# Optimization experiments

Hardware: AMD Instinct MI355X
Metric: run time of the kernel (lower is better)

The kernel has to match this reference:

```python
import jax, jax.numpy as jnp
import numpy as np

N = 20000   # nodes per frame
T = 16      # frames
E = 320000  # edges per frame
C = 128     # in_channels
H = 128     # hidden_channels
P = 100000  # decode pairs


def setup_inputs() -> dict:
    key = jax.random.key(0)
    ks = jax.random.split(key, 12)
    s = 1.0 / np.sqrt(H)
    return {
        "x_seq": jax.random.normal(ks[0], (T, N, C), jnp.float32),
        "edge_index": jax.random.randint(ks[1], (T, 2, E), 0, N, jnp.int32),
        "edge_pairs": jax.random.randint(ks[2], (2, P), 0, N, jnp.int32),
        "W1": jax.random.normal(ks[3], (C, H), jnp.float32) * s,
        "b1": jnp.zeros((H,), jnp.float32),
        "W2": jax.random.normal(ks[4], (H, H), jnp.float32) * s,
        "b2": jnp.zeros((H,), jnp.float32),
        "W3": jax.random.normal(ks[5], (H, H), jnp.float32) * s,
        "b3": jnp.zeros((H,), jnp.float32),
        "w_ih": jax.random.normal(ks[6], (3 * H, H), jnp.float32) * s,
        "w_hh": jax.random.normal(ks[7], (3 * H, H), jnp.float32) * s,
        "b_ih": jnp.zeros((3 * H,), jnp.float32),
        "b_hh": jnp.zeros((3 * H,), jnp.float32),
    }


def _gcn(x, src, dst, W, b):
    # PyG GCNConv: h = x @ W; add self-loops; D^{-1/2}(A+I)D^{-1/2} aggregation; + b
    h = x @ W                                   # [N, H]
    ones = jnp.ones(src.shape[0], x.dtype)
    deg = jax.ops.segment_sum(ones, dst, num_segments=N) + 1.0  # self-loop included
    dinv = jax.lax.rsqrt(deg)
    norm = dinv[src] * dinv[dst]                # [E]
    agg = jax.ops.segment_sum(h[src] * norm[:, None], dst, num_segments=N)
    agg = agg + h * (dinv * dinv)[:, None]      # self-loop message (norm = 1/deg)
    return agg + b


def reference(x_seq, edge_index, edge_pairs, W1, b1, W2, b2, W3, b3,
              w_ih, w_hh, b_ih, b_hh):
    def frame(_, inp):
        x, ei = inp
        src, dst = ei[0], ei[1]
        h = jax.nn.relu(_gcn(x, src, dst, W1, b1))
        h = jax.nn.relu(_gcn(h, src, dst, W2, b2))
        h = _gcn(h, src, dst, W3, b3)
        return None, h

    _, feats = jax.lax.scan(frame, None, (x_seq, edge_index))  # [T, N, H]

    # single-layer torch GRU over time; only final hidden state needed
    def gru_step(hprev, x_t):
        gi = x_t @ w_ih.T + b_ih                # [N, 3H]
        gh = hprev @ w_hh.T + b_hh
        i_r, i_z, i_n = jnp.split(gi, 3, axis=1)
        h_r, h_z, h_n = jnp.split(gh, 3, axis=1)
        r = jax.nn.sigmoid(i_r + h_r)
        z = jax.nn.sigmoid(i_z + h_z)
        n = jnp.tanh(i_n + r * h_n)
        h_new = (1.0 - z) * n + z * hprev
        return h_new, None

    h0 = jnp.zeros((N, H), x_seq.dtype)
    h_last, _ = jax.lax.scan(gru_step, h0, feats)  # [N, H]

    zs = h_last[edge_pairs[0]]                  # [P, H]
    zd = h_last[edge_pairs[1]]
    return jnp.sum(zs * zd, axis=1)             # [P]
```

## Files before the change

### kernel.cpp

```cpp
#include <hip/hip_runtime.h>
#include <hip/hip_bf16.h>

#define NN 20000
#define TT 16
#define EE 320000
#define CC 128
#define HH 128
#define PP 100000
#define QN (NN / 4)

typedef float  f32x4  __attribute__((ext_vector_type(4)));
typedef unsigned short ushort8v __attribute__((ext_vector_type(8)));
typedef unsigned u32x4 __attribute__((ext_vector_type(4)));
typedef _Float16 h2v __attribute__((ext_vector_type(2)));
typedef _Float16 h4v __attribute__((ext_vector_type(4)));
typedef _Float16 f16x8 __attribute__((ext_vector_type(8)));

union pk16 { unsigned u; _Float16 h[2]; };


__global__ void hist_all_k(const int* __restrict__ edge_index, int* __restrict__ cnt_all) {
    int b = blockIdx.x;
    int f = b & 15, chunk = b >> 4;
    const int* dst = edge_index + (size_t)f * 2 * EE + EE;
    int* cnt = cnt_all + f * NN;
    int base = chunk * 1024 + threadIdx.x;
#pragma unroll
    for (int i = 0; i < 4; ++i) {
        int e = base + i * 256;
        if (e < EE) {
            int d = __builtin_nontemporal_load(dst + e);
            atomicAdd(&cnt[d], 1);
        }
    }
}

__global__ __launch_bounds__(1024) void scan_all_k(const int* __restrict__ cnt_all,
                                                   int* __restrict__ offs_all,
                                                   float* __restrict__ dinv_all,
                                                   int* __restrict__ cursor_all) {
    __shared__ int part[1024];
    int f = blockIdx.x;
    const int* cnt = cnt_all + f * NN;
    int* offs = offs_all + f * (NN + 1);
    int t = threadIdx.x;
    int base = t * 20;
    int vals[20];
    int s = 0;
#pragma unroll
    for (int i = 0; i < 20; ++i) {
        int idx = base + i;
        int v = (idx < NN) ? cnt[idx] : 0;
        vals[i] = v; s += v;
    }
    part[t] = s;
    __syncthreads();
    for (int off = 1; off < 1024; off <<= 1) {
        int v = (t >= off) ? part[t - off] : 0;
        __syncthreads();
        part[t] += v;
        __syncthreads();
    }
    int run = part[t] - s;
#pragma unroll
    for (int i = 0; i < 20; ++i) {
        int idx = base + i;
        if (idx < NN) {
            offs[idx] = run;
            cursor_all[f * NN + idx] = f * EE + run;
            dinv_all[f * NN + idx] = rsqrtf((float)vals[i] + 1.0f);
            run += vals[i];
        }
    }
    if (t == 0) offs[NN] = EE;
}

__global__ void fill_all_k(const int* __restrict__ edge_index,
                           int* __restrict__ cursor_all,
                           unsigned short* __restrict__ csr_all) {
    int b = blockIdx.x;
    int f = b & 15, chunk = b >> 4;
    const int* src = edge_index + (size_t)f * 2 * EE;
    const int* dst = src + EE;
    int* cur = cursor_all + f * NN;
    int base = chunk * 1024 + threadIdx.x;
#pragma unroll
    for (int i = 0; i < 4; ++i) {
        int e = base + i * 256;
        if (e < EE) {
            int d = __builtin_nontemporal_load(dst + e);
            int s = __builtin_nontemporal_load(src + e);
            int pos = atomicAdd(&cur[d], 1);
            csr_all[pos] = (unsigned short)s;
        }
    }
}

__global__ void wprep_t_k(const float* __restrict__ W,
                          _Float16* __restrict__ oh,
                          _Float16* __restrict__ ol) {
    int i = blockIdx.x * blockDim.x + threadIdx.x;
    if (i >= 128 * 128) return;
    int n = i >> 7, k = i & 127;
    float v = W[k * 128 + n];
    _Float16 h = (_Float16)v;
    oh[i] = h;
    ol[i] = (_Float16)(v - (float)h);
}

__global__ __launch_bounds__(256) void wprep_p_k(const float* __restrict__ wsrc,
                                                 _Float16* __restrict__ oh,
                                                 _Float16* __restrict__ ol) {
    int u = blockIdx.x * blockDim.x + threadIdx.x;
    if (u >= 6144) return;
    int lane = u & 63, q = (u >> 6) & 3, wv = (u >> 8) & 7, g = u >> 11;
    int lm = lane & 15, lq = lane >> 4;
    const float* s = wsrc + (size_t)(g * 128 + wv * 16 + lm) * 128 + q * 32 + lq * 8;
#pragma unroll
    for (int e = 0; e < 8; ++e) {
        float v = s[e];
        _Float16 h = (_Float16)v;
        oh[(size_t)u * 8 + e] = h;
        ol[(size_t)u * 8 + e] = (_Float16)(v - (float)h);
    }
}

__global__ __launch_bounds__(256) void scale_k(const float* __restrict__ x,
                                               const float* __restrict__ dinv_all,
                                               _Float16* __restrict__ g) {
    int idx = blockIdx.x * blockDim.x + threadIdx.x;
    int row = idx >> 5, q = idx & 31;
    const f32x4* xp = (const f32x4*)(x + (size_t)row * 128 + q * 4);
    f32x4 v = __builtin_nontemporal_load(xp);
    float d = dinv_all[row];
    h4v o;
    o.x = (_Float16)(v.x * d); o.y = (_Float16)(v.y * d);
    o.z = (_Float16)(v.z * d); o.w = (_Float16)(v.w * d);
    *(h4v*)(g + (size_t)row * 128 + q * 4) = o;
}

__global__ __launch_bounds__(128) void agg_half_k(const _Float16* __restrict__ g,
                                                  const unsigned short* __restrict__ csr_all,
                                                  const int* __restrict__ offs_all,
                                                  _Float16* __restrict__ a) {
    int b = blockIdx.x;
    int xcd = b & 7;
    int r1 = b >> 3;
    int grp = r1 % QN;
    int pass = r1 / QN;
    int f = xcd + ((pass & 1) << 3);
    int hoff = (pass >> 1) * 64;
    int t = threadIdx.x;
    int node = grp * 4 + (t >> 5);
    int lane = t & 31;
    const int* offs = offs_all + f * (NN + 1);
    const unsigned short* csr = csr_all + (size_t)f * EE;
    const _Float16* gf = g + (size_t)f * NN * HH + hoff + lane * 2;
    int beg = offs[node], end = offs[node + 1];
    float a0 = 0.f, a1 = 0.f;
    int e = beg;
    for (; e + 3 < end; e += 4) {
        int s0 = csr[e], s1 = csr[e + 1], s2 = csr[e + 2], s3 = csr[e + 3];
        h2v v0 = *(const h2v*)(gf + (size_t)s0 * HH);
        h2v v1 = *(const h2v*)(gf + (size_t)s1 * HH);
        h2v v2 = *(const h2v*)(gf + (size_t)s2 * HH);
        h2v v3 = *(const h2v*)(gf + (size_t)s3 * HH);
        a0 += ((float)v0.x + (float)v1.x) + ((float)v2.x + (float)v3.x);
        a1 += ((float)v0.y + (float)v1.y) + ((float)v2.y + (float)v3.y);
    }
    for (; e < end; ++e) {
        h2v v = *(const h2v*)(gf + (size_t)csr[e] * HH);
        a0 += (float)v.x; a1 += (float)v.y;
    }
    h2v vs = *(const h2v*)(gf + (size_t)node * HH);
    a0 += (float)vs.x; a1 += (float)vs.y;
    h2v r; r.x = (_Float16)a0; r.y = (_Float16)a1;
    *(h2v*)(a + ((size_t)f * NN + node) * HH + hoff + lane * 2) = r;
}

__global__ __launch_bounds__(256) void gemm_f16(const _Float16* __restrict__ A,
                                                const _Float16* __restrict__ Bh,
                                                const _Float16* __restrict__ Bl,
                                                _Float16* __restrict__ out,
                                                const float* __restrict__ rowscale,
                                                const float* __restrict__ bias,
                                                int M, int NC, int relu, int postscale) {
    __shared__ _Float16 As[64 * 72], Bhs[64 * 72], Bls[64 * 72];
    int t = threadIdx.x;
    int b = blockIdx.x;
    int xcd = b & 7, k = b >> 3;
    int row_t = xcd + ((k >> 1) << 3);
    int col_t = k & 1;
    int row0 = row_t * 64, col0 = col_t * 64;
    int w = t >> 6, lane = t & 63;
    int wm = (w & 1) * 32, wn = (w >> 1) * 32;
    int lm = lane & 15, lq = lane >> 4;
    f32x4 acc[2][2] = {};

    for (int ks = 0; ks < 2; ++ks) {
        if (ks) __syncthreads();
#pragma unroll
        for (int p = 0; p < 2; ++p) {
            int s = t + p * 256;
            int r = s >> 3, c8 = s & 7;
            int gr = row0 + r;
            ushort8v va = {};
            if (gr < M)
                va = *(const ushort8v*)(A + (size_t)gr * 128 + ks * 64 + c8 * 8);
            *(ushort8v*)&As[r * 72 + c8 * 8] = va;
            *(ushort8v*)&Bhs[r * 72 + c8 * 8] =
                *(const ushort8v*)(Bh + (size_t)(col0 + r) * 128 + ks * 64 + c8 * 8);
            *(ushort8v*)&Bls[r * 72 + c8 * 8] =
                *(const ushort8v*)(Bl + (size_t)(col0 + r) * 128 + ks * 64 + c8 * 8);
        }
        __syncthreads();
#pragma unroll
        for (int q = 0; q < 2; ++q) {
            int ko = q * 32 + lq * 8;
            f16x8 av[2], bh[2], bl[2];
#pragma unroll
            for (int i = 0; i < 2; ++i)
                av[i] = *(const f16x8*)&As[(wm + i * 16 + lm) * 72 + ko];
#pragma unroll
            for (int j = 0; j < 2; ++j) {
                bh[j] = *(const f16x8*)&Bhs[(wn + j * 16 + lm) * 72 + ko];
                bl[j] = *(const f16x8*)&Bls[(wn + j * 16 + lm) * 72 + ko];
            }
#pragma unroll
            for (int i = 0; i < 2; ++i)
#pragma unroll
                for (int j = 0; j < 2; ++j) {
                    acc[i][j] = __builtin_amdgcn_mfma_f32_16x16x32_f16(av[i], bh[j], acc[i][j], 0, 0, 0);
                    acc[i][j] = __builtin_amdgcn_mfma_f32_16x16x32_f16(av[i], bl[j], acc[i][j], 0, 0, 0);
                }
        }
    }
#pragma unroll
    for (int i = 0; i < 2; ++i)
#pragma unroll
        for (int reg = 0; reg < 4; ++reg) {
            int gr = row0 + wm + i * 16 + lq * 4 + reg;
            if (gr < M) {
                float sc = rowscale ? rowscale[gr] : 1.0f;
#pragma unroll
                for (int j = 0; j < 2; ++j) {
                    int col = col0 + wn + j * 16 + lm;
                    float v = acc[i][j][reg];
                    if (rowscale) v *= sc;
                    v += bias[col];
                    if (relu) v = fmaxf(v, 0.f);
                    if (postscale) v *= sc;
                    out[(size_t)gr * NC + col] = (_Float16)v;
                }
            }
        }
}

__global__ __launch_bounds__(512, 1) void gru_all_k(const _Float16* __restrict__ F,
                                                    const _Float16* __restrict__ wihh,
                                                    const _Float16* __restrict__ wihl,
                                                    const _Float16* __restrict__ whhh,
                                                    const _Float16* __restrict__ whhl,
                                                    const float* __restrict__ b_ih,
                                                    const float* __restrict__ b_hh,
                                                    float* __restrict__ hgru) {
    __shared__ unsigned hsu[8192];
    __shared__ _Float16 fsu[8192];
    int t = threadIdx.x;
    int row0 = blockIdx.x * 64;
    for (int s = t; s < 8192; s += 512) hsu[s] = 0u;

    int w = t >> 6, lane = t & 63;
    int lm = lane & 15, lq = lane >> 4;
    int h_idx = w * 16 + lm;
    float bsr = b_ih[h_idx] + b_hh[h_idx];
    float bsz = b_ih[h_idx + 128] + b_hh[h_idx + 128];
    float bni = b_ih[h_idx + 256];
    float bnh = b_hh[h_idx + 256];
    size_t wb = (size_t)w * 2048 + (size_t)lane * 8;
    int qv = h_idx >> 5, lqv = (h_idx >> 3) & 3, ev = h_idx & 7;

    for (int tt = 0; tt < TT; ++tt) {
        __syncthreads();
        const _Float16* Ft = F + ((size_t)tt * NN + row0) * 128;
#pragma unroll
        for (int it = 0; it < 2; ++it) {
            int s = t + it * 512;
            int r = s >> 4, c8 = s & 15;
            ushort8v val = {};
            if (row0 + r < NN)
                val = *(const ushort8v*)(Ft + (size_t)r * 128 + c8 * 8);
            int fu = ((r >> 4) * 4 + (c8 >> 2)) * 64 + (c8 & 3) * 16 + (r & 15);
            *(ushort8v*)(fsu + fu * 8) = val;
        }
        __syncthreads();

        f32x4 accr[4], accz[4], accni[4], accnh[4];
#pragma unroll
        for (int i = 0; i < 4; ++i) {
            accr[i] = (f32x4){0.f, 0.f, 0.f, 0.f};
            accz[i] = (f32x4){0.f, 0.f, 0.f, 0.f};
            accni[i] = (f32x4){0.f, 0.f, 0.f, 0.f};
            accnh[i] = (f32x4){0.f, 0.f, 0.f, 0.f};
        }

#pragma unroll
        for (int q = 0; q < 4; ++q) {
            size_t o = wb + q * 512;
            f16x8 wr_h = *(const f16x8*)(wihh + o);
            f16x8 wr_l = *(const f16x8*)(wihl + o);
            f16x8 wz_h = *(const f16x8*)(wihh + o + 16384);
            f16x8 wz_l = *(const f16x8*)(wihl + o + 16384);
            f16x8 wn_h = *(const f16x8*)(wihh + o + 32768);
            f16x8 wn_l = *(const f16x8*)(wihl + o + 32768);
#pragma unroll
            for (int i = 0; i < 4; ++i) {
                f16x8 af = *(const f16x8*)(fsu + ((i * 4 + q) * 64 + lane) * 8);
                accr[i]  = __builtin_amdgcn_mfma_f32_16x16x32_f16(af, wr_h, accr[i], 0, 0, 0);
                accr[i]  = __builtin_amdgcn_mfma_f32_16x16x32_f16(af, wr_l, accr[i], 0, 0, 0);
                accz[i]  = __builtin_amdgcn_mfma_f32_16x16x32_f16(af, wz_h, accz[i], 0, 0, 0);
                accz[i]  = __builtin_amdgcn_mfma_f32_16x16x32_f16(af, wz_l, accz[i], 0, 0, 0);
                accni[i] = __builtin_amdgcn_mfma_f32_16x16x32_f16(af, wn_h, accni[i], 0, 0, 0);
                accni[i] = __builtin_amdgcn_mfma_f32_16x16x32_f16(af, wn_l, accni[i], 0, 0, 0);
            }
        }

#pragma unroll
        for (int q = 0; q < 4; ++q) {
            size_t o = wb + q * 512;
            f16x8 wr_h = *(const f16x8*)(whhh + o);
            f16x8 wr_l = *(const f16x8*)(whhl + o);
            f16x8 wz_h = *(const f16x8*)(whhh + o + 16384);
            f16x8 wz_l = *(const f16x8*)(whhl + o + 16384);
            f16x8 wn_h = *(const f16x8*)(whhh + o + 32768);
            f16x8 wn_l = *(const f16x8*)(whhl + o + 32768);
#pragma unroll
            for (int i = 0; i < 4; ++i) {
                const unsigned* hp = hsu + ((i * 4 + q) * 64 + lane) * 8;
                u32x4 v0 = *(const u32x4*)(hp);
                u32x4 v1 = *(const u32x4*)(hp + 4);
                f16x8 ah, al;
#pragma unroll
                for (int e = 0; e < 4; ++e) {
                    pk16 c; c.u = v0[e]; ah[e] = c.h[0]; al[e] = c.h[1];
                    pk16 d; d.u = v1[e]; ah[e + 4] = d.h[0]; al[e + 4] = d.h[1];
                }
                accr[i]  = __builtin_amdgcn_mfma_f32_16x16x32_f16(ah, wr_h, accr[i], 0, 0, 0);
                accr[i]  = __builtin_amdgcn_mfma_f32_16x16x32_f16(ah, wr_l, accr[i], 0, 0, 0);
                accr[i]  = __builtin_amdgcn_mfma_f32_16x16x32_f16(al, wr_h, accr[i], 0, 0, 0);
                accz[i]  = __builtin_amdgcn_mfma_f32_16x16x32_f16(ah, wz_h, accz[i], 0, 0, 0);
                accz[i]  = __builtin_amdgcn_mfma_f32_16x16x32_f16(ah, wz_l, accz[i], 0, 0, 0);
                accz[i]  = __builtin_amdgcn_mfma_f32_16x16x32_f16(al, wz_h, accz[i], 0, 0, 0);
                accnh[i] = __builtin_amdgcn_mfma_f32_16x16x32_f16(ah, wn_h, accnh[i], 0, 0, 0);
                accnh[i] = __builtin_amdgcn_mfma_f32_16x16x32_f16(ah, wn_l, accnh[i], 0, 0, 0);
                accnh[i] = __builtin_amdgcn_mfma_f32_16x16x32_f16(al, wn_h, accnh[i], 0, 0, 0);
            }
        }

#pragma unroll
        for (int i = 0; i < 4; ++i)
#pragma unroll
            for (int reg = 0; reg < 4; ++reg) {
                int u = (i * 4 + qv) * 64 + lqv * 16 + lq * 4 + reg;
                pk16 c; c.u = hsu[u * 8 + ev];
                float hp = (float)c.h[0] + (float)c.h[1];
                float r = 1.f / (1.f + __expf(-(accr[i][reg] + bsr)));
                float z = 1.f / (1.f + __expf(-(accz[i][reg] + bsz)));
                float nv = tanhf(accni[i][reg] + bni + r * (accnh[i][reg] + bnh));
                accr[i][reg] = (1.f - z) * nv + z * hp;
            }
        __syncthreads();
#pragma unroll
        for (int i = 0; i < 4; ++i)
#pragma unroll
            for (int reg = 0; reg < 4; ++reg) {
                int u = (i * 4 + qv) * 64 + lqv * 16 + lq * 4 + reg;
                float hv = accr[i][reg];
                _Float16 hi = (_Float16)hv;
                pk16 c; c.h[0] = hi; c.h[1] = (_Float16)(hv - (float)hi);
                hsu[u * 8 + ev] = c.u;
                if (tt == TT - 1) {
                    int gr = row0 + i * 16 + lq * 4 + reg;
                    if (gr < NN) hgru[(size_t)gr * 128 + h_idx] = hv;
                }
            }
    }
}

__global__ __launch_bounds__(256) void decode_k(const float* __restrict__ hgru,
                                                const int* __restrict__ pairs,
                                                float* __restrict__ out) {
    int gid = blockIdx.x * blockDim.x + threadIdx.x;
    int w = gid >> 6;
    int lane = threadIdx.x & 63;
    if (w >= PP) return;
    int s = pairs[w], d = pairs[PP + w];
    const float* zs = hgru + (size_t)s * HH;
    const float* zd = hgru + (size_t)d * HH;
    float acc = zs[lane] * zd[lane] + zs[lane + 64] * zd[lane + 64];
#pragma unroll
    for (int off = 32; off > 0; off >>= 1) acc += __shfl_down(acc, off);
    if (lane == 0) out[w] = acc;
}

static inline size_t align256(size_t x) { return (x + 255) & ~(size_t)255; }

extern "C" void kernel_launch(void* const* d_in, const int* in_sizes, int n_in,
                              void* d_out, int out_size, void* d_ws, size_t ws_size,
                              hipStream_t stream) {
    const float* x_seq      = (const float*)d_in[0];
    const int*   edge_index = (const int*)d_in[1];
    const int*   edge_pairs = (const int*)d_in[2];
    const float* W1 = (const float*)d_in[3];
    const float* b1 = (const float*)d_in[4];
    const float* W2 = (const float*)d_in[5];
    const float* b2 = (const float*)d_in[6];
    const float* W3 = (const float*)d_in[7];
    const float* b3 = (const float*)d_in[8];
    const float* w_ih = (const float*)d_in[9];
    const float* w_hh = (const float*)d_in[10];
    const float* b_ih = (const float*)d_in[11];
    const float* b_hh = (const float*)d_in[12];

    const size_t MALL = (size_t)TT * NN;

    char* p = (char*)d_ws;
    int*   cnt_all    = (int*)p;   p += align256(MALL * sizeof(int));
    int*   offs_all   = (int*)p;   p += align256((size_t)TT * (NN + 1) * sizeof(int));
    int*   cursor_all = (int*)p;   p += align256(MALL * sizeof(int));
    float* dinv_all   = (float*)p; p += align256(MALL * sizeof(float));
    unsigned short* csr_all = (unsigned short*)p; p += align256((size_t)TT * EE * sizeof(unsigned short));
    _Float16* g   = (_Float16*)p;  p += align256(MALL * HH * sizeof(_Float16));
    _Float16* a   = (_Float16*)p;  p += align256(MALL * HH * sizeof(_Float16));
    _Float16* F   = (_Float16*)p;  p += align256(MALL * HH * sizeof(_Float16));
    float* hgru = (float*)p;       p += align256((size_t)NN * HH * sizeof(float));
    _Float16* W1h = (_Float16*)p; p += align256(128 * 128 * 2);
    _Float16* W1l = (_Float16*)p; p += align256(128 * 128 * 2);
    _Float16* W2h = (_Float16*)p; p += align256(128 * 128 * 2);
    _Float16* W2l = (_Float16*)p; p += align256(128 * 128 * 2);
    _Float16* W3h = (_Float16*)p; p += align256(128 * 128 * 2);
    _Float16* W3l = (_Float16*)p; p += align256(128 * 128 * 2);
    _Float16* wihh = (_Float16*)p; p += align256(384 * 128 * 2);
    _Float16* wihl = (_Float16*)p; p += align256(384 * 128 * 2);
    _Float16* whhh = (_Float16*)p; p += align256(384 * 128 * 2);
    _Float16* whhl = (_Float16*)p; p += align256(384 * 128 * 2);

    hipMemsetAsync(cnt_all, 0, MALL * sizeof(int), stream);

    wprep_t_k<<<64, 256, 0, stream>>>(W1, W1h, W1l);
    wprep_t_k<<<64, 256, 0, stream>>>(W2, W2h, W2l);
    wprep_t_k<<<64, 256, 0, stream>>>(W3, W3h, W3l);
    wprep_p_k<<<24, 256, 0, stream>>>(w_ih, wihh, wihl);
    wprep_p_k<<<24, 256, 0, stream>>>(w_hh, whhh, whhl);

    int ge = ((EE + 1023) / 1024) * TT;
    hist_all_k<<<ge, 256, 0, stream>>>(edge_index, cnt_all);
    scan_all_k<<<TT, 1024, 0, stream>>>(cnt_all, offs_all, dinv_all, cursor_all);
    fill_all_k<<<ge, 256, 0, stream>>>(edge_index, cursor_all, csr_all);

    scale_k<<<(int)(MALL * 32 / 256), 256, 0, stream>>>(x_seq, dinv_all, g);

    int gagg = 8 * QN * 4;
    int ggemm = 2 * (int)(MALL / 64);

    agg_half_k<<<gagg, 128, 0, stream>>>(g, csr_all, offs_all, a);
    gemm_f16<<<ggemm, 256, 0, stream>>>(a, W1h, W1l, g, dinv_all, b1, (int)MALL, 128, 1, 1);
    agg_half_k<<<gagg, 128, 0, stream>>>(g, csr_all, offs_all, a);
    gemm_f16<<<ggemm, 256, 0, stream>>>(a, W2h, W2l, g, dinv_all, b2, (int)MALL, 128, 1, 1);
    agg_half_k<<<gagg, 128, 0, stream>>>(g, csr_all, offs_all, a);
    gemm_f16<<<ggemm, 256, 0, stream>>>(a, W3h, W3l, F, dinv_all, b3, (int)MALL, 128, 0, 0);

    int gru_blocks = (NN + 63) / 64;
    gru_all_k<<<gru_blocks, 512, 0, stream>>>(F, wihh, wihl, whhh, whhl,
                                              b_ih, b_hh, hgru);

    decode_k<<<(PP * 64 + 255) / 256, 256, 0, stream>>>(hgru, edge_pairs, (float*)d_out);
}
```

Before: 1.728 ms.

## Restructure GRU kernel: 32-row blocks, double-buffered LDS, prefetch, swizzle

Rewrites the fused GRU kernel so each block handles 32 rows instead of 64, which doubles the number of blocks for better CU coverage. The F tile for the next timestep is prefetched into registers while the current step computes. The hidden-state hi/lo halves go into separate double-buffered LDS arrays with an XOR swizzle, so one of the two per-step barriers can go. The previous hidden state stays in registers instead of being re-read from LDS. The cost is that the weight fragments are reloaded from global memory twice as often across blocks, and the bounds checks are removed because the code assumes NN is divisible by 32.

```diff
diff --git a/kernel.cpp b/kernel.cpp
--- a/kernel.cpp
+++ b/kernel.cpp
@@ -15,8 +15,6 @@
 typedef _Float16 h2v __attribute__((ext_vector_type(2)));
 typedef _Float16 h4v __attribute__((ext_vector_type(4)));
 typedef _Float16 f16x8 __attribute__((ext_vector_type(8)));
-
-union pk16 { unsigned u; _Float16 h[2]; };
 
 
 __global__ void hist_all_k(const int* __restrict__ edge_index, int* __restrict__ cnt_all) {
@@ -264,11 +262,15 @@
                                                     const float* __restrict__ b_ih,
                                                     const float* __restrict__ b_hh,
                                                     float* __restrict__ hgru) {
-    __shared__ unsigned hsu[8192];
-    __shared__ _Float16 fsu[8192];
+    __shared__ _Float16 fsu[2][4096];
+    __shared__ _Float16 hsh[2][4096];
+    __shared__ _Float16 hsl[2][4096];
     int t = threadIdx.x;
-    int row0 = blockIdx.x * 64;
-    for (int s = t; s < 8192; s += 512) hsu[s] = 0u;
+    int row0 = blockIdx.x * 32;
+    for (int s = t; s < 4096; s += 512) {
+        hsh[0][s] = (_Float16)0.f;
+        hsl[0][s] = (_Float16)0.f;
+    }
 
     int w = t >> 6, lane = t & 63;
     int lm = lane & 15, lq = lane >> 4;
@@ -278,26 +280,27 @@
     float bni = b_ih[h_idx + 256];
     float bnh = b_hh[h_idx + 256];
     size_t wb = (size_t)w * 2048 + (size_t)lane * 8;
+
+    int sr = t >> 4, sc = t & 15;
+    int sofs = (((((sr >> 4) * 4 + (sc >> 2)) * 64) + (sc & 3) * 16 + (sr & 15)) * 8)
+               ^ ((sc & 3) << 3);
+    const _Float16* Fg = F + ((size_t)row0 + sr) * 128 + sc * 8;
+
     int qv = h_idx >> 5, lqv = (h_idx >> 3) & 3, ev = h_idx & 7;
 
+    float hprev[2][4] = {};
+    ushort8v vF = *(const ushort8v*)(Fg);
+
     for (int tt = 0; tt < TT; ++tt) {
+        int cur = tt & 1, nxt = cur ^ 1;
+        *(ushort8v*)&fsu[cur][sofs] = vF;
         __syncthreads();
-        const _Float16* Ft = F + ((size_t)tt * NN + row0) * 128;
-#pragma unroll
-        for (int it = 0; it < 2; ++it) {
-            int s = t + it * 512;
-            int r = s >> 4, c8 = s & 15;
-            ushort8v val = {};
-            if (row0 + r < NN)
-                val = *(const ushort8v*)(Ft + (size_t)r * 128 + c8 * 8);
-            int fu = ((r >> 4) * 4 + (c8 >> 2)) * 64 + (c8 & 3) * 16 + (r & 15);
-            *(ushort8v*)(fsu + fu * 8) = val;
-        }
-        __syncthreads();
-
-        f32x4 accr[4], accz[4], accni[4], accnh[4];
-#pragma unroll
-        for (int i = 0; i < 4; ++i) {
+        if (tt + 1 < TT)
+            vF = *(const ushort8v*)(Fg + (size_t)(tt + 1) * NN * 128);
+
+        f32x4 accr[2], accz[2], accni[2], accnh[2];
+#pragma unroll
+        for (int i = 0; i < 2; ++i) {
             accr[i] = (f32x4){0.f, 0.f, 0.f, 0.f};
             accz[i] = (f32x4){0.f, 0.f, 0.f, 0.f};
             accni[i] = (f32x4){0.f, 0.f, 0.f, 0.f};
@@ -314,8 +317,8 @@
             f16x8 wn_h = *(const f16x8*)(wihh + o + 32768);
             f16x8 wn_l = *(const f16x8*)(wihl + o + 32768);
 #pragma unroll
-            for (int i = 0; i < 4; ++i) {
-                f16x8 af = *(const f16x8*)(fsu + ((i * 4 + q) * 64 + lane) * 8);
+            for (int i = 0; i < 2; ++i) {
+                f16x8 af = *(const f16x8*)&fsu[cur][((((i * 4 + q) * 64 + lane) * 8)) ^ (lq << 3)];
                 accr[i]  = __builtin_amdgcn_mfma_f32_16x16x32_f16(af, wr_h, accr[i], 0, 0, 0);
                 accr[i]  = __builtin_amdgcn_mfma_f32_16x16x32_f16(af, wr_l, accr[i], 0, 0, 0);
                 accz[i]  = __builtin_amdgcn_mfma_f32_16x16x32_f16(af, wz_h, accz[i], 0, 0, 0);
@@ -335,16 +338,10 @@
             f16x8 wn_h = *(const f16x8*)(whhh + o + 32768);
             f16x8 wn_l = *(const f16x8*)(whhl + o + 32768);
 #pragma unroll
-            for (int i = 0; i < 4; ++i) {
-                const unsigned* hp = hsu + ((i * 4 + q) * 64 + lane) * 8;
-                u32x4 v0 = *(const u32x4*)(hp);
-                u32x4 v1 = *(const u32x4*)(hp + 4);
-                f16x8 ah, al;
-#pragma unroll
-                for (int e = 0; e < 4; ++e) {
-                    pk16 c; c.u = v0[e]; ah[e] = c.h[0]; al[e] = c.h[1];
-                    pk16 d; d.u = v1[e]; ah[e + 4] = d.h[0]; al[e + 4] = d.h[1];
-                }
+            for (int i = 0; i < 2; ++i) {
+                int fofs = ((((i * 4 + q) * 64 + lane) * 8)) ^ (lq << 3);
+                f16x8 ah = *(const f16x8*)&hsh[cur][fofs];
+                f16x8 al = *(const f16x8*)&hsl[cur][fofs];
                 accr[i]  = __builtin_amdgcn_mfma_f32_16x16x32_f16(ah, wr_h, accr[i], 0, 0, 0);
                 accr[i]  = __builtin_amdgcn_mfma_f32_16x16x32_f16(ah, wr_l, accr[i], 0, 0, 0);
                 accr[i]  = __builtin_amdgcn_mfma_f32_16x16x32_f16(al, wr_h, accr[i], 0, 0, 0);
@@ -358,31 +355,21 @@
         }
 
 #pragma unroll
-        for (int i = 0; i < 4; ++i)
+        for (int i = 0; i < 2; ++i)
 #pragma unroll
             for (int reg = 0; reg < 4; ++reg) {
-                int u = (i * 4 + qv) * 64 + lqv * 16 + lq * 4 + reg;
-                pk16 c; c.u = hsu[u * 8 + ev];
-                float hp = (float)c.h[0] + (float)c.h[1];
                 float r = 1.f / (1.f + __expf(-(accr[i][reg] + bsr)));
                 float z = 1.f / (1.f + __expf(-(accz[i][reg] + bsz)));
                 float nv = tanhf(accni[i][reg] + bni + r * (accnh[i][reg] + bnh));
-                accr[i][reg] = (1.f - z) * nv + z * hp;
-            }
-        __syncthreads();
-#pragma unroll
-        for (int i = 0; i < 4; ++i)
-#pragma unroll
-            for (int reg = 0; reg < 4; ++reg) {
-                int u = (i * 4 + qv) * 64 + lqv * 16 + lq * 4 + reg;
-                float hv = accr[i][reg];
+                float hv = (1.f - z) * nv + z * hprev[i][reg];
+                hprev[i][reg] = hv;
                 _Float16 hi = (_Float16)hv;
-                pk16 c; c.h[0] = hi; c.h[1] = (_Float16)(hv - (float)hi);
-                hsu[u * 8 + ev] = c.u;
-                if (tt == TT - 1) {
-                    int gr = row0 + i * 16 + lq * 4 + reg;
-                    if (gr < NN) hgru[(size_t)gr * 128 + h_idx] = hv;
-                }
+                _Float16 lo = (_Float16)(hv - (float)hi);
+                int u = ((((i * 4 + qv) * 64 + lqv * 16 + lq * 4 + reg) * 8 + ev)) ^ (lqv << 3);
+                hsh[nxt][u] = hi;
+                hsl[nxt][u] = lo;
+                if (tt == TT - 1)
+                    hgru[(size_t)(row0 + i * 16 + lq * 4 + reg) * 128 + h_idx] = hv;
             }
     }
 }
@@ -470,7 +457,7 @@
     agg_half_k<<<gagg, 128, 0, stream>>>(g, csr_all, offs_all, a);
     gemm_f16<<<ggemm, 256, 0, stream>>>(a, W3h, W3l, F, dinv_all, b3, (int)MALL, 128, 0, 0);
 
-    int gru_blocks = (NN + 63) / 64;
+    int gru_blocks = NN / 32;
     gru_all_k<<<gru_blocks, 512, 0, stream>>>(F, wihh, wihl, whhh, whhl,
                                               b_ih, b_hh, hgru);
 
```

Result: slower. 1.811 ms (+4.8%).
